# Performance work log

Hardware: AMD Instinct MI355X
Metric: run time of the kernel (lower is better)

The kernel has to match this reference:

```python
import jax, jax.numpy as jnp
import numpy as np
from jax import lax

SIZE = 64
N_PHASES = SIZE * (SIZE - 1) // 2  # 2016
LOSS_DB_CM = 0.5
INSERTION_LOSS_DB = LOSS_DB_CM * 0.1          # per-MZI insertion loss (dB)
LOSS_AMP = 10.0 ** (-INSERTION_LOSS_DB / 20.0)  # amplitude transmission per MZI
NONLINEAR_COEFF = 2.6e-20

# Reck triangular mesh ordering: layer i = 1..SIZE-1, MZIs on adjacent modes (j, j+1)
_MODE_IDX = np.array([j for i in range(1, SIZE) for j in range(i)], dtype=np.int32)


def build_mesh_unitary(phases):
    """Sequentially compose 2x2 MZI rotations into a SIZE x SIZE complex matrix.
    Each MZI with phase theta applies T = loss * [[cos, i sin],[i sin, cos]] to
    adjacent modes (m, m+1). U = T_K ... T_1."""
    U0 = jnp.eye(SIZE, dtype=jnp.complex64)

    def step(U, xs):
        theta, m = xs
        c = jnp.cos(theta).astype(jnp.complex64)
        s = (1j * jnp.sin(theta)).astype(jnp.complex64)
        row_a = U[m]
        row_b = U[m + 1]
        new_a = LOSS_AMP * (c * row_a + s * row_b)
        new_b = LOSS_AMP * (s * row_a + c * row_b)
        U = U.at[m].set(new_a).at[m + 1].set(new_b)
        return U, None

    U, _ = lax.scan(step, U0, (phases, jnp.asarray(_MODE_IDX)))
    return U


def setup_inputs() -> dict:
    key = jax.random.key(0)
    k1, k2, k3 = jax.random.split(key, 3)
    B = 262144
    x_real = jax.random.normal(k1, (B, SIZE), dtype=jnp.float32)
    x_imag = jax.random.normal(k2, (B, SIZE), dtype=jnp.float32)
    # nn.initializers.uniform(scale=2*pi) -> U[0, 2*pi)
    phases = jax.random.uniform(k3, (N_PHASES,), dtype=jnp.float32) * (2.0 * np.pi)
    return {"x_real": x_real, "x_imag": x_imag, "phases": phases}


def reference(x_real, x_imag, phases):
    x = (x_real + 1j * x_imag).astype(jnp.complex64)  # [B, SIZE]
    U = build_mesh_unitary(phases)                    # [SIZE, SIZE] complex64
    # vmapped mesh apply == batched matmul with the composed unitary
    out = x @ U.T                                     # [B, SIZE]
    # Kerr nonlinearity (include_nonlinearity=True)
    optical_power = jnp.abs(out) ** 2
    nonlinear_phase = NONLINEAR_COEFF * optical_power * 1000.0
    out = out * jnp.exp(1j * nonlinear_phase.astype(jnp.complex64))
    return out
```

## Files before the change

kernel.cpp:

```cpp
#include <hip/hip_runtime.h>


#define PSIZE 64
#define N_PHASES 2016
#define NLAYER 63
#define LOSS_AMP 0.99426007f
#define NL_COEFF 2.6e-17f

#define UF32_BYTES (2 * PSIZE * PSIZE * 4)
#define WSPLIT_BYTES (4 * PSIZE * PSIZE * 2)
#define WS_NEED (UF32_BYTES + WSPLIT_BYTES)

typedef __attribute__((ext_vector_type(8))) short sh8;
typedef __attribute__((ext_vector_type(4))) float f32x4;

__device__ __align__(16) float g_U_fallback[2 * PSIZE * PSIZE];

__device__ inline unsigned short f32_to_bf16_rn(float f) {
  unsigned int u = __float_as_uint(f);
  u += 0x7fffu + ((u >> 16) & 1u);
  return (unsigned short)(u >> 16);
}
__device__ inline float bf16_to_f32(unsigned short h) {
  return __uint_as_float(((unsigned int)h) << 16);
}

__device__ inline float rdlane(float v, int l) {
  return __int_as_float(__builtin_amdgcn_readlane(__float_as_int(v), l));
}

__device__ inline unsigned pkbf16(float a, float b) {
  unsigned r;
  asm("v_cvt_pk_bf16_f32 %0, %1, %2" : "=v"(r) : "v"(a), "v"(b));
  return r;
}
__device__ inline float lo16f(unsigned u) { return __uint_as_float(u << 16); }
__device__ inline float hi16f(unsigned u) {
  return __uint_as_float(u & 0xFFFF0000u);
}
__device__ inline sh8 mk8(unsigned a, unsigned b, unsigned c, unsigned d) {
  union { unsigned u[4]; sh8 s; } t;
  t.u[0] = a; t.u[1] = b; t.u[2] = c; t.u[3] = d;
  return t.s;
}

__global__ __launch_bounds__(512, 1) void build_kernel(
    const float* __restrict__ phases,
    float* __restrict__ Uf32,
    unsigned short* __restrict__ Wout) {
  __shared__ float2 sS[3][PSIZE * PSIZE];
  __shared__ float2 sWsm[PSIZE * PSIZE];
  const int tid = threadIdx.x;
  const int wv = tid >> 6;
  const int lane = tid & 63;

  for (int idx = tid; idx < PSIZE * PSIZE; idx += 512) {
    const int li = idx >> 6;
    const int m = idx & 63;
    float2 w = make_float2(1.0f, 0.0f);
    if (li < NLAYER && m <= li) {
      const float th = phases[(li * (li + 1)) / 2 + m];
      w = make_float2(LOSS_AMP * cosf(th), LOSS_AMP * sinf(th));
    }
    sWsm[idx] = w;
  }
  __syncthreads();

  float ure[PSIZE], uim[PSIZE];
  if (wv < 4) {
#pragma unroll
    for (int r = 0; r < PSIZE; ++r) {
      ure[r] = (r == lane) ? 1.0f : 0.0f;
      uim[r] = 0.0f;
    }
    for (int l = 0; l < 16; ++l) {
      const int li = wv * 16 + l;
      const float2 w2 = sWsm[li * 64 + lane];
#pragma unroll
      for (int m = 0; m < NLAYER; ++m) {
        const float wc = rdlane(w2.x, m);
        const float ws = rdlane(w2.y, m);
        const float are = ure[m], aim = uim[m];
        const float bre = ure[m + 1], bim = uim[m + 1];
        ure[m]     = fmaf(wc, are, -ws * bim);
        uim[m]     = fmaf(wc, aim,  ws * bre);
        ure[m + 1] = fmaf(wc, bre, -ws * aim);
        uim[m + 1] = fmaf(wc, bim,  ws * are);
      }
    }
  }
  __syncthreads();

  if (wv < 4) {
    float2* dst = (wv == 3) ? sWsm : sS[wv];
#pragma unroll
    for (int r = 0; r < PSIZE; ++r)
      dst[r * 64 + lane] = make_float2(ure[r], uim[r]);
  }
  __syncthreads();

  const int wg = wv >> 2;
  const int w4 = wv & 3;
  {
    const float2* A  = (wg == 0) ? sS[1] : sWsm;
    const float2* Bm = (wg == 0) ? sS[0] : sS[2];
    float pre[16], pim[16];
#pragma unroll
    for (int r = 0; r < 16; ++r) { pre[r] = 0.f; pim[r] = 0.f; }
    for (int m = 0; m < PSIZE; ++m) {
      const float2 b = Bm[m * 64 + lane];
#pragma unroll
      for (int r = 0; r < 16; ++r) {
        const float2 a = A[(16 * w4 + r) * 64 + m];
        pre[r] = fmaf(a.x, b.x, fmaf(-a.y, b.y, pre[r]));
        pim[r] = fmaf(a.x, b.y, fmaf( a.y, b.x, pim[r]));
      }
    }
    __syncthreads();
    float2* Pd = (wg == 0) ? sS[0] : sS[1];
#pragma unroll
    for (int r = 0; r < 16; ++r)
      Pd[(16 * w4 + r) * 64 + lane] = make_float2(pre[r], pim[r]);
  }
  __syncthreads();

  float fre[8], fim[8];
#pragma unroll
  for (int r = 0; r < 8; ++r) { fre[r] = 0.f; fim[r] = 0.f; }
  for (int m = 0; m < PSIZE; ++m) {
    const float2 b = sS[0][m * 64 + lane];
#pragma unroll
    for (int r = 0; r < 8; ++r) {
      const float2 a = sS[1][(8 * wv + r) * 64 + m];
      fre[r] = fmaf(a.x, b.x, fmaf(-a.y, b.y, fre[r]));
      fim[r] = fmaf(a.x, b.y, fmaf( a.y, b.x, fim[r]));
    }
  }

  float* Udst = (Uf32 != nullptr) ? Uf32 : g_U_fallback;
#pragma unroll
  for (int r = 0; r < 8; ++r) {
    const int rr = 8 * wv + r;
    ((float2*)Udst)[rr * 64 + lane] = make_float2(fre[r], fim[r]);
  }
  if (Wout != nullptr) {
    const int slot = lane >> 3, kin = lane & 7;
#pragma unroll
    for (int r = 0; r < 8; ++r) {
      const int n = 8 * wv + r;
      const int base = n * 64 + ((slot ^ (n & 7)) << 3) + kin;
      const unsigned short rh = f32_to_bf16_rn(fre[r]);
      const unsigned short rl = f32_to_bf16_rn(fre[r] - bf16_to_f32(rh));
      const unsigned short ih = f32_to_bf16_rn(fim[r]);
      const unsigned short il = f32_to_bf16_rn(fim[r] - bf16_to_f32(ih));
      Wout[0 * 4096 + base] = rh;
      Wout[1 * 4096 + base] = rl;
      Wout[2 * 4096 + base] = ih;
      Wout[3 * 4096 + base] = il;
    }
  }
}

__global__ __launch_bounds__(256, 2) void apply_mfma(
    const unsigned short* __restrict__ W,
    const float* __restrict__ xr,
    const float* __restrict__ xi,
    float* __restrict__ out_re,
    float* __restrict__ out_im) {
  __shared__ __align__(16) unsigned short sW[4 * PSIZE * PSIZE];
  {
    const float4* src = (const float4*)W;
    float4* dst = (float4*)sW;
    for (int i = threadIdx.x; i < WSPLIT_BYTES / 16; i += 256) dst[i] = src[i];
  }
  __syncthreads();

  const int lane = threadIdx.x & 63;
  const int wave = threadIdx.x >> 6;
  const int lm = lane & 15;
  const int lg = lane >> 4;
  const long row0 = (long)blockIdx.x * 128 + (long)wave * 32;

  f32x4 accRe[2][4], accIm[2][4];
#pragma unroll
  for (int a = 0; a < 2; ++a)
#pragma unroll
    for (int b = 0; b < 4; ++b) {
      accRe[a][b] = f32x4{0.f, 0.f, 0.f, 0.f};
      accIm[a][b] = f32x4{0.f, 0.f, 0.f, 0.f};
    }

#pragma unroll
  for (int ks = 0; ks < 2; ++ks) {
    sh8 arh[2], arl[2], aih[2], ail[2], anh[2], anl[2];
#pragma unroll
    for (int mt = 0; mt < 2; ++mt) {
      const long r = row0 + mt * 16 + lm;
      const float4* pr = (const float4*)(xr + r * PSIZE + ks * 32 + lg * 8);
      const float4* pi = (const float4*)(xi + r * PSIZE + ks * 32 + lg * 8);
      const float4 v0 = pr[0], v1 = pr[1];
      const float4 w0 = pi[0], w1 = pi[1];

      const unsigned rh0 = pkbf16(v0.x, v0.y), rh1 = pkbf16(v0.z, v0.w);
      const unsigned rh2 = pkbf16(v1.x, v1.y), rh3 = pkbf16(v1.z, v1.w);
      const unsigned rl0 = pkbf16(v0.x - lo16f(rh0), v0.y - hi16f(rh0));
      const unsigned rl1 = pkbf16(v0.z - lo16f(rh1), v0.w - hi16f(rh1));
      const unsigned rl2 = pkbf16(v1.x - lo16f(rh2), v1.y - hi16f(rh2));
      const unsigned rl3 = pkbf16(v1.z - lo16f(rh3), v1.w - hi16f(rh3));
      arh[mt] = mk8(rh0, rh1, rh2, rh3);
      arl[mt] = mk8(rl0, rl1, rl2, rl3);

      const unsigned ih0 = pkbf16(w0.x, w0.y), ih1 = pkbf16(w0.z, w0.w);
      const unsigned ih2 = pkbf16(w1.x, w1.y), ih3 = pkbf16(w1.z, w1.w);
      const unsigned il0 = pkbf16(w0.x - lo16f(ih0), w0.y - hi16f(ih0));
      const unsigned il1 = pkbf16(w0.z - lo16f(ih1), w0.w - hi16f(ih1));
      const unsigned il2 = pkbf16(w1.x - lo16f(ih2), w1.y - hi16f(ih2));
      const unsigned il3 = pkbf16(w1.z - lo16f(ih3), w1.w - hi16f(ih3));
      aih[mt] = mk8(ih0, ih1, ih2, ih3);
      ail[mt] = mk8(il0, il1, il2, il3);
      anh[mt] = mk8(ih0 ^ 0x80008000u, ih1 ^ 0x80008000u,
                    ih2 ^ 0x80008000u, ih3 ^ 0x80008000u);
      anl[mt] = mk8(il0 ^ 0x80008000u, il1 ^ 0x80008000u,
                    il2 ^ 0x80008000u, il3 ^ 0x80008000u);
    }

#pragma unroll
    for (int nt = 0; nt < 4; ++nt) {
      const int n = nt * 16 + lm;
      const int sidx = n * 64 + (((ks * 4 + lg) ^ (n & 7)) << 3);
      const sh8 bRh = *(const sh8*)&sW[0 * 4096 + sidx];
      const sh8 bRl = *(const sh8*)&sW[1 * 4096 + sidx];
      const sh8 bIh = *(const sh8*)&sW[2 * 4096 + sidx];
      const sh8 bIl = *(const sh8*)&sW[3 * 4096 + sidx];
#pragma unroll
      for (int mt = 0; mt < 2; ++mt) {
        f32x4 cr = accRe[mt][nt];
        cr = __builtin_amdgcn_mfma_f32_16x16x32_bf16(arh[mt], bRh, cr, 0, 0, 0);
        cr = __builtin_amdgcn_mfma_f32_16x16x32_bf16(arh[mt], bRl, cr, 0, 0, 0);
        cr = __builtin_amdgcn_mfma_f32_16x16x32_bf16(arl[mt], bRh, cr, 0, 0, 0);
        cr = __builtin_amdgcn_mfma_f32_16x16x32_bf16(anh[mt], bIh, cr, 0, 0, 0);
        cr = __builtin_amdgcn_mfma_f32_16x16x32_bf16(anh[mt], bIl, cr, 0, 0, 0);
        cr = __builtin_amdgcn_mfma_f32_16x16x32_bf16(anl[mt], bIh, cr, 0, 0, 0);
        accRe[mt][nt] = cr;
        f32x4 ci = accIm[mt][nt];
        ci = __builtin_amdgcn_mfma_f32_16x16x32_bf16(arh[mt], bIh, ci, 0, 0, 0);
        ci = __builtin_amdgcn_mfma_f32_16x16x32_bf16(arh[mt], bIl, ci, 0, 0, 0);
        ci = __builtin_amdgcn_mfma_f32_16x16x32_bf16(arl[mt], bIh, ci, 0, 0, 0);
        ci = __builtin_amdgcn_mfma_f32_16x16x32_bf16(aih[mt], bRh, ci, 0, 0, 0);
        ci = __builtin_amdgcn_mfma_f32_16x16x32_bf16(aih[mt], bRl, ci, 0, 0, 0);
        ci = __builtin_amdgcn_mfma_f32_16x16x32_bf16(ail[mt], bRh, ci, 0, 0, 0);
        accIm[mt][nt] = ci;
      }
    }
  }

#pragma unroll
  for (int mt = 0; mt < 2; ++mt) {
#pragma unroll
    for (int reg = 0; reg < 4; ++reg) {
      const long row = row0 + mt * 16 + lg * 4 + reg;
#pragma unroll
      for (int nt = 0; nt < 4; ++nt) {
        const int col = nt * 16 + lm;
        const float re = accRe[mt][nt][reg];
        const float im = accIm[mt][nt][reg];
        const float p = NL_COEFF * fmaf(re, re, im * im);
        out_re[row * PSIZE + col] = fmaf(-im, p, re);
        if (out_im != nullptr) out_im[row * PSIZE + col] = fmaf(re, p, im);
      }
    }
  }
}

__global__ __launch_bounds__(256, 2) void tail_kernel(
    const float* __restrict__ Usrc,
    const float* __restrict__ xr,
    const float* __restrict__ xi,
    float* __restrict__ out_re,
    float* __restrict__ out_im,
    long rowStart, long nrows) {
  __shared__ __align__(16) float sU[2 * PSIZE * PSIZE];
  {
    const float4* g4 = (const float4*)((Usrc != nullptr) ? Usrc : g_U_fallback);
    float4* s4 = (float4*)sU;
    for (int i = threadIdx.x; i < (2 * PSIZE * PSIZE) / 4; i += 256)
      s4[i] = g4[i];
  }
  __syncthreads();

  const long row = rowStart + (long)blockIdx.x * 256 + threadIdx.x;
  if (row >= nrows) return;

  const float4* xr4 = (const float4*)(xr + (size_t)row * PSIZE);
  const float4* xi4 = (const float4*)(xi + (size_t)row * PSIZE);

  float aR[PSIZE], aI[PSIZE];
#pragma unroll
  for (int j = 0; j < PSIZE; ++j) { aR[j] = 0.0f; aI[j] = 0.0f; }

  const float4* su4 = (const float4*)sU;

#pragma unroll 1
  for (int kc = 0; kc < 8; ++kc) {
    const float4 a0 = xr4[2 * kc];
    const float4 a1 = xr4[2 * kc + 1];
    const float4 b0 = xi4[2 * kc];
    const float4 b1 = xi4[2 * kc + 1];
    const float4* up = su4 + kc * 4;
#pragma unroll
    for (int j = 0; j < PSIZE; ++j) {
      const float4 u0 = up[j * 32 + 0];
      const float4 u1 = up[j * 32 + 1];
      const float4 u2 = up[j * 32 + 2];
      const float4 u3 = up[j * 32 + 3];
      float r = aR[j], m = aI[j];
      r = fmaf(a0.x, u0.x, r); r = fmaf(-b0.x, u0.y, r);
      m = fmaf(a0.x, u0.y, m); m = fmaf( b0.x, u0.x, m);
      r = fmaf(a0.y, u0.z, r); r = fmaf(-b0.y, u0.w, r);
      m = fmaf(a0.y, u0.w, m); m = fmaf( b0.y, u0.z, m);
      r = fmaf(a0.z, u1.x, r); r = fmaf(-b0.z, u1.y, r);
      m = fmaf(a0.z, u1.y, m); m = fmaf( b0.z, u1.x, m);
      r = fmaf(a0.w, u1.z, r); r = fmaf(-b0.w, u1.w, r);
      m = fmaf(a0.w, u1.w, m); m = fmaf( b0.w, u1.z, m);
      r = fmaf(a1.x, u2.x, r); r = fmaf(-b1.x, u2.y, r);
      m = fmaf(a1.x, u2.y, m); m = fmaf( b1.x, u2.x, m);
      r = fmaf(a1.y, u2.z, r); r = fmaf(-b1.y, u2.w, r);
      m = fmaf(a1.y, u2.w, m); m = fmaf( b1.y, u2.z, m);
      r = fmaf(a1.z, u3.x, r); r = fmaf(-b1.z, u3.y, r);
      m = fmaf(a1.z, u3.y, m); m = fmaf( b1.z, u3.x, m);
      r = fmaf(a1.w, u3.z, r); r = fmaf(-b1.w, u3.w, r);
      m = fmaf(a1.w, u3.w, m); m = fmaf( b1.w, u3.z, m);
      aR[j] = r; aI[j] = m;
    }
  }

  float* orp = out_re + (size_t)row * PSIZE;
  float* oip = (out_im != nullptr) ? (out_im + (size_t)row * PSIZE) : nullptr;
#pragma unroll
  for (int jq = 0; jq < 16; ++jq) {
    const int j = 4 * jq;
    float4 vr, vi;
    {
      const float p = NL_COEFF * fmaf(aR[j], aR[j], aI[j] * aI[j]);
      vr.x = fmaf(-aI[j], p, aR[j]); vi.x = fmaf(aR[j], p, aI[j]);
    }
    {
      const float p = NL_COEFF * fmaf(aR[j+1], aR[j+1], aI[j+1] * aI[j+1]);
      vr.y = fmaf(-aI[j+1], p, aR[j+1]); vi.y = fmaf(aR[j+1], p, aI[j+1]);
    }
    {
      const float p = NL_COEFF * fmaf(aR[j+2], aR[j+2], aI[j+2] * aI[j+2]);
      vr.z = fmaf(-aI[j+2], p, aR[j+2]); vi.z = fmaf(aR[j+2], p, aI[j+2]);
    }
    {
      const float p = NL_COEFF * fmaf(aR[j+3], aR[j+3], aI[j+3] * aI[j+3]);
      vr.w = fmaf(-aI[j+3], p, aR[j+3]); vi.w = fmaf(aR[j+3], p, aI[j+3]);
    }
    ((float4*)orp)[jq] = vr;
    if (oip != nullptr) ((float4*)oip)[jq] = vi;
  }
}

extern "C" void kernel_launch(void* const* d_in, const int* in_sizes, int n_in,
                              void* d_out, int out_size, void* d_ws, size_t ws_size,
                              hipStream_t stream) {
  int pidx = -1;
  for (int i = 0; i < n_in; ++i) {
    if (in_sizes[i] == N_PHASES) { pidx = i; break; }
  }
  if (pidx < 0) pidx = 2;
  int xa = -1, xb = -1;
  for (int i = 0; i < n_in; ++i) {
    if (i == pidx) continue;
    if (xa < 0) xa = i;
    else if (xb < 0) xb = i;
  }
  if (xa < 0 || xb < 0) return;

  const float* phases = (const float*)d_in[pidx];
  const float* x_real = (const float*)d_in[xa];
  const float* x_imag = (const float*)d_in[xb];

  long b_in = (long)in_sizes[xa] / PSIZE;
  if ((long)in_sizes[xb] / PSIZE < b_in) b_in = (long)in_sizes[xb] / PSIZE;

  float* out = (float*)d_out;
  float* out_re = out;
  float* out_im = nullptr;
  long nrows;

  if ((long)out_size >= 2 * b_in * PSIZE) {
    const long half = (long)out_size / 2;
    out_im = out + half;
    long cap = half / PSIZE;
    nrows = (b_in < cap) ? b_in : cap;
  } else {
    long cap = (long)out_size / PSIZE;
    nrows = (b_in < cap) ? b_in : cap;
  }
  if (nrows <= 0) return;

  float* Uf32 = nullptr;
  unsigned short* Wsplit = nullptr;
  if (d_ws != nullptr && ws_size >= (size_t)WS_NEED) {
    Uf32 = (float*)d_ws;
    Wsplit = (unsigned short*)((char*)d_ws + UF32_BYTES);
  }

  build_kernel<<<1, 512, 0, stream>>>(phases, Uf32, Wsplit);

  const long ntiles = (Wsplit != nullptr) ? (nrows / 128) : 0;
  if (ntiles > 0) {
    apply_mfma<<<(int)ntiles, 256, 0, stream>>>(Wsplit, x_real, x_imag,
                                                out_re, out_im);
  }
  const long done = ntiles * 128;
  if (done < nrows) {
    const long rem = nrows - done;
    const int tblocks = (int)((rem + 255) / 256);
    tail_kernel<<<tblocks, 256, 0, stream>>>(Uf32, x_real, x_imag,
                                             out_re, out_im, done, nrows);
  }
}
```

Baseline: 231.7 us.

## Fuse unitary build into apply kernel with ticket-based producer/consumer handoff

Replaces the separate single-block build kernel and the MFMA apply kernel with one persistent-style launch. The first block to take a ticket builds the unitary, publishes the split bf16 weights through global memory with a release flag, then does its own tile. All other blocks spin on the flag before loading the weights. This removes a kernel launch boundary and the serial gap before apply starts. In exchange it adds a memset, spin-waiting blocks that occupy CUs while the build runs, and a reliance on the ticket holder being scheduled.

```diff
diff --git a/kernel.cpp b/kernel.cpp
--- a/kernel.cpp
+++ b/kernel.cpp
@@ -7,9 +7,9 @@
 #define LOSS_AMP 0.99426007f
 #define NL_COEFF 2.6e-17f
 
-#define UF32_BYTES (2 * PSIZE * PSIZE * 4)
 #define WSPLIT_BYTES (4 * PSIZE * PSIZE * 2)
-#define WS_NEED (UF32_BYTES + WSPLIT_BYTES)
+#define CTRL_BYTES 256
+#define FUSED_WS_NEED (CTRL_BYTES + WSPLIT_BYTES)
 
 typedef __attribute__((ext_vector_type(8))) short sh8;
 typedef __attribute__((ext_vector_type(4))) float f32x4;
@@ -24,11 +24,9 @@
 __device__ inline float bf16_to_f32(unsigned short h) {
   return __uint_as_float(((unsigned int)h) << 16);
 }
-
 __device__ inline float rdlane(float v, int l) {
   return __int_as_float(__builtin_amdgcn_readlane(__float_as_int(v), l));
 }
-
 __device__ inline unsigned pkbf16(float a, float b) {
   unsigned r;
   asm("v_cvt_pk_bf16_f32 %0, %1, %2" : "=v"(r) : "v"(a), "v"(b));
@@ -44,38 +42,46 @@
   return t.s;
 }
 
-__global__ __launch_bounds__(512, 1) void build_kernel(
+__global__ __launch_bounds__(256, 2) void fused_kernel(
     const float* __restrict__ phases,
-    float* __restrict__ Uf32,
-    unsigned short* __restrict__ Wout) {
-  __shared__ float2 sS[3][PSIZE * PSIZE];
-  __shared__ float2 sWsm[PSIZE * PSIZE];
+    const float* __restrict__ xr,
+    const float* __restrict__ xi,
+    float* __restrict__ out_re,
+    float* __restrict__ out_im,
+    unsigned* __restrict__ ctrl,
+    unsigned short* __restrict__ Wg,
+    long nrows) {
+  __shared__ __align__(16) float2 sA[PSIZE * PSIZE];
+  __shared__ __align__(16) float2 sB[PSIZE * PSIZE];
+  __shared__ unsigned s_ticket;
+  unsigned short* sW = (unsigned short*)sA;
+
   const int tid = threadIdx.x;
-  const int wv = tid >> 6;
-  const int lane = tid & 63;
-
-  for (int idx = tid; idx < PSIZE * PSIZE; idx += 512) {
-    const int li = idx >> 6;
-    const int m = idx & 63;
-    float2 w = make_float2(1.0f, 0.0f);
-    if (li < NLAYER && m <= li) {
-      const float th = phases[(li * (li + 1)) / 2 + m];
-      w = make_float2(LOSS_AMP * cosf(th), LOSS_AMP * sinf(th));
-    }
-    sWsm[idx] = w;
-  }
+  if (tid == 0) s_ticket = atomicAdd(&ctrl[0], 1u);
   __syncthreads();
 
-  float ure[PSIZE], uim[PSIZE];
-  if (wv < 4) {
+  if (s_ticket == 0) {
+    const int wv = tid >> 6, lane = tid & 63;
+
+    for (int idx = tid; idx < PSIZE * PSIZE; idx += 256) {
+      const int li = idx >> 6, m = idx & 63;
+      float2 w = make_float2(1.0f, 0.0f);
+      if (li < NLAYER && m <= li) {
+        const float th = phases[(li * (li + 1)) / 2 + m];
+        w = make_float2(LOSS_AMP * cosf(th), LOSS_AMP * sinf(th));
+      }
+      sA[idx] = w;
+    }
+    __syncthreads();
+
+    float ure[PSIZE], uim[PSIZE];
 #pragma unroll
     for (int r = 0; r < PSIZE; ++r) {
       ure[r] = (r == lane) ? 1.0f : 0.0f;
       uim[r] = 0.0f;
     }
     for (int l = 0; l < 16; ++l) {
-      const int li = wv * 16 + l;
-      const float2 w2 = sWsm[li * 64 + lane];
+      const float2 w2 = sA[(wv * 16 + l) * 64 + lane];
 #pragma unroll
       for (int m = 0; m < NLAYER; ++m) {
         const float wc = rdlane(w2.x, m);
@@ -88,92 +94,122 @@
         uim[m + 1] = fmaf(wc, bim,  ws * are);
       }
     }
-  }
-  __syncthreads();
-
-  if (wv < 4) {
-    float2* dst = (wv == 3) ? sWsm : sS[wv];
-#pragma unroll
-    for (int r = 0; r < PSIZE; ++r)
-      dst[r * 64 + lane] = make_float2(ure[r], uim[r]);
-  }
-  __syncthreads();
-
-  const int wg = wv >> 2;
-  const int w4 = wv & 3;
-  {
-    const float2* A  = (wg == 0) ? sS[1] : sWsm;
-    const float2* Bm = (wg == 0) ? sS[0] : sS[2];
+    __syncthreads();
+
+    if (wv == 3) {
+#pragma unroll
+      for (int r = 0; r < PSIZE; ++r)
+        ((float2*)Wg)[r * 64 + lane] = make_float2(ure[r], uim[r]);
+    }
+    if (wv == 0) {
+#pragma unroll
+      for (int r = 0; r < PSIZE; ++r)
+        sA[r * 64 + lane] = make_float2(ure[r], uim[r]);
+    }
+    if (wv == 1) {
+#pragma unroll
+      for (int r = 0; r < PSIZE; ++r)
+        sB[r * 64 + lane] = make_float2(ure[r], uim[r]);
+    }
+    __syncthreads();
+
     float pre[16], pim[16];
 #pragma unroll
     for (int r = 0; r < 16; ++r) { pre[r] = 0.f; pim[r] = 0.f; }
     for (int m = 0; m < PSIZE; ++m) {
-      const float2 b = Bm[m * 64 + lane];
+      const float2 b = sA[m * 64 + lane];
 #pragma unroll
       for (int r = 0; r < 16; ++r) {
-        const float2 a = A[(16 * w4 + r) * 64 + m];
+        const float2 a = sB[(wv * 16 + r) * 64 + m];
         pre[r] = fmaf(a.x, b.x, fmaf(-a.y, b.y, pre[r]));
         pim[r] = fmaf(a.x, b.y, fmaf( a.y, b.x, pim[r]));
       }
     }
     __syncthreads();
-    float2* Pd = (wg == 0) ? sS[0] : sS[1];
+    if (wv == 2) {
+#pragma unroll
+      for (int r = 0; r < PSIZE; ++r)
+        sA[r * 64 + lane] = make_float2(ure[r], uim[r]);
+    }
 #pragma unroll
     for (int r = 0; r < 16; ++r)
-      Pd[(16 * w4 + r) * 64 + lane] = make_float2(pre[r], pim[r]);
-  }
-  __syncthreads();
-
-  float fre[8], fim[8];
-#pragma unroll
-  for (int r = 0; r < 8; ++r) { fre[r] = 0.f; fim[r] = 0.f; }
-  for (int m = 0; m < PSIZE; ++m) {
-    const float2 b = sS[0][m * 64 + lane];
-#pragma unroll
-    for (int r = 0; r < 8; ++r) {
-      const float2 a = sS[1][(8 * wv + r) * 64 + m];
-      fre[r] = fmaf(a.x, b.x, fmaf(-a.y, b.y, fre[r]));
-      fim[r] = fmaf(a.x, b.y, fmaf( a.y, b.x, fim[r]));
-    }
-  }
-
-  float* Udst = (Uf32 != nullptr) ? Uf32 : g_U_fallback;
-#pragma unroll
-  for (int r = 0; r < 8; ++r) {
-    const int rr = 8 * wv + r;
-    ((float2*)Udst)[rr * 64 + lane] = make_float2(fre[r], fim[r]);
-  }
-  if (Wout != nullptr) {
+      sB[(wv * 16 + r) * 64 + lane] = make_float2(pre[r], pim[r]);
+    __syncthreads();
+
+#pragma unroll
+    for (int r = 0; r < 16; ++r) { pre[r] = 0.f; pim[r] = 0.f; }
+    for (int m = 0; m < PSIZE; ++m) {
+      const float2 b = sB[m * 64 + lane];
+#pragma unroll
+      for (int r = 0; r < 16; ++r) {
+        const float2 a = sA[(wv * 16 + r) * 64 + m];
+        pre[r] = fmaf(a.x, b.x, fmaf(-a.y, b.y, pre[r]));
+        pim[r] = fmaf(a.x, b.y, fmaf( a.y, b.x, pim[r]));
+      }
+    }
+    __syncthreads();
+#pragma unroll
+    for (int r = 0; r < 16; ++r)
+      sB[(wv * 16 + r) * 64 + lane] = make_float2(pre[r], pim[r]);
+    for (int idx = tid; idx < PSIZE * PSIZE; idx += 256)
+      sA[idx] = ((const float2*)Wg)[idx];
+    __syncthreads();
+
+    float fre[16], fim[16];
+#pragma unroll
+    for (int r = 0; r < 16; ++r) { fre[r] = 0.f; fim[r] = 0.f; }
+    for (int m = 0; m < PSIZE; ++m) {
+      const float2 b = sB[m * 64 + lane];
+#pragma unroll
+      for (int r = 0; r < 16; ++r) {
+        const float2 a = sA[(wv * 16 + r) * 64 + m];
+        fre[r] = fmaf(a.x, b.x, fmaf(-a.y, b.y, fre[r]));
+        fim[r] = fmaf(a.x, b.y, fmaf( a.y, b.x, fim[r]));
+      }
+    }
+    __syncthreads();
+
     const int slot = lane >> 3, kin = lane & 7;
 #pragma unroll
-    for (int r = 0; r < 8; ++r) {
-      const int n = 8 * wv + r;
+    for (int r = 0; r < 16; ++r) {
+      const int n = wv * 16 + r;
       const int base = n * 64 + ((slot ^ (n & 7)) << 3) + kin;
       const unsigned short rh = f32_to_bf16_rn(fre[r]);
       const unsigned short rl = f32_to_bf16_rn(fre[r] - bf16_to_f32(rh));
       const unsigned short ih = f32_to_bf16_rn(fim[r]);
       const unsigned short il = f32_to_bf16_rn(fim[r] - bf16_to_f32(ih));
-      Wout[0 * 4096 + base] = rh;
-      Wout[1 * 4096 + base] = rl;
-      Wout[2 * 4096 + base] = ih;
-      Wout[3 * 4096 + base] = il;
-    }
-  }
-}
-
-__global__ __launch_bounds__(256, 2) void apply_mfma(
-    const unsigned short* __restrict__ W,
-    const float* __restrict__ xr,
-    const float* __restrict__ xi,
-    float* __restrict__ out_re,
-    float* __restrict__ out_im) {
-  __shared__ __align__(16) unsigned short sW[4 * PSIZE * PSIZE];
-  {
-    const float4* src = (const float4*)W;
-    float4* dst = (float4*)sW;
-    for (int i = threadIdx.x; i < WSPLIT_BYTES / 16; i += 256) dst[i] = src[i];
-  }
-  __syncthreads();
+      sW[0 * 4096 + base] = rh;
+      sW[1 * 4096 + base] = rl;
+      sW[2 * 4096 + base] = ih;
+      sW[3 * 4096 + base] = il;
+    }
+    __syncthreads();
+    {
+      const float4* s4 = (const float4*)sW;
+      float4* d4 = (float4*)Wg;
+      for (int i = tid; i < WSPLIT_BYTES / 16; i += 256) d4[i] = s4[i];
+    }
+    __syncthreads();
+    __threadfence();
+    if (tid == 0)
+      __hip_atomic_store(&ctrl[1], 1u, __ATOMIC_RELEASE,
+                         __HIP_MEMORY_SCOPE_AGENT);
+  } else {
+    if (tid == 0) {
+      while (__hip_atomic_load(&ctrl[1], __ATOMIC_RELAXED,
+                               __HIP_MEMORY_SCOPE_AGENT) == 0u)
+        __builtin_amdgcn_s_sleep(16);
+    }
+    __syncthreads();
+    (void)__hip_atomic_load(&ctrl[1], __ATOMIC_ACQUIRE,
+                            __HIP_MEMORY_SCOPE_AGENT);
+    {
+      const float4* src = (const float4*)Wg;
+      float4* dst = (float4*)sW;
+      for (int i = tid; i < WSPLIT_BYTES / 16; i += 256) dst[i] = src[i];
+    }
+    __syncthreads();
+  }
 
   const int lane = threadIdx.x & 63;
   const int wave = threadIdx.x >> 6;
@@ -195,7 +231,8 @@
     sh8 arh[2], arl[2], aih[2], ail[2], anh[2], anl[2];
 #pragma unroll
     for (int mt = 0; mt < 2; ++mt) {
-      const long r = row0 + mt * 16 + lm;
+      long r = row0 + mt * 16 + lm;
+      if (r >= nrows) r = nrows - 1;
       const float4* pr = (const float4*)(xr + r * PSIZE + ks * 32 + lg * 8);
       const float4* pi = (const float4*)(xi + r * PSIZE + ks * 32 + lg * 8);
       const float4 v0 = pr[0], v1 = pr[1];
@@ -259,36 +296,129 @@
 #pragma unroll
     for (int reg = 0; reg < 4; ++reg) {
       const long row = row0 + mt * 16 + lg * 4 + reg;
-#pragma unroll
-      for (int nt = 0; nt < 4; ++nt) {
-        const int col = nt * 16 + lm;
-        const float re = accRe[mt][nt][reg];
-        const float im = accIm[mt][nt][reg];
-        const float p = NL_COEFF * fmaf(re, re, im * im);
-        out_re[row * PSIZE + col] = fmaf(-im, p, re);
-        if (out_im != nullptr) out_im[row * PSIZE + col] = fmaf(re, p, im);
-      }
-    }
-  }
+      if (row < nrows) {
+#pragma unroll
+        for (int nt = 0; nt < 4; ++nt) {
+          const int col = nt * 16 + lm;
+          const float re = accRe[mt][nt][reg];
+          const float im = accIm[mt][nt][reg];
+          const float p = NL_COEFF * fmaf(re, re, im * im);
+          out_re[row * PSIZE + col] = fmaf(-im, p, re);
+          if (out_im != nullptr) out_im[row * PSIZE + col] = fmaf(re, p, im);
+        }
+      }
+    }
+  }
+}
+
+__global__ __launch_bounds__(512, 1) void build_kernel(
+    const float* __restrict__ phases) {
+  __shared__ float2 sS[3][PSIZE * PSIZE];
+  __shared__ float2 sWsm[PSIZE * PSIZE];
+  const int tid = threadIdx.x;
+  const int wv = tid >> 6;
+  const int lane = tid & 63;
+
+  for (int idx = tid; idx < PSIZE * PSIZE; idx += 512) {
+    const int li = idx >> 6, m = idx & 63;
+    float2 w = make_float2(1.0f, 0.0f);
+    if (li < NLAYER && m <= li) {
+      const float th = phases[(li * (li + 1)) / 2 + m];
+      w = make_float2(LOSS_AMP * cosf(th), LOSS_AMP * sinf(th));
+    }
+    sWsm[idx] = w;
+  }
+  __syncthreads();
+
+  float ure[PSIZE], uim[PSIZE];
+  if (wv < 4) {
+#pragma unroll
+    for (int r = 0; r < PSIZE; ++r) {
+      ure[r] = (r == lane) ? 1.0f : 0.0f;
+      uim[r] = 0.0f;
+    }
+    for (int l = 0; l < 16; ++l) {
+      const float2 w2 = sWsm[(wv * 16 + l) * 64 + lane];
+#pragma unroll
+      for (int m = 0; m < NLAYER; ++m) {
+        const float wc = rdlane(w2.x, m);
+        const float ws = rdlane(w2.y, m);
+        const float are = ure[m], aim = uim[m];
+        const float bre = ure[m + 1], bim = uim[m + 1];
+        ure[m]     = fmaf(wc, are, -ws * bim);
+        uim[m]     = fmaf(wc, aim,  ws * bre);
+        ure[m + 1] = fmaf(wc, bre, -ws * aim);
+        uim[m + 1] = fmaf(wc, bim,  ws * are);
+      }
+    }
+  }
+  __syncthreads();
+  if (wv < 4) {
+    float2* dst = (wv == 3) ? sWsm : sS[wv];
+#pragma unroll
+    for (int r = 0; r < PSIZE; ++r)
+      dst[r * 64 + lane] = make_float2(ure[r], uim[r]);
+  }
+  __syncthreads();
+
+  const int wg = wv >> 2, w4 = wv & 3;
+  {
+    const float2* A  = (wg == 0) ? sS[1] : sWsm;
+    const float2* Bm = (wg == 0) ? sS[0] : sS[2];
+    float pre[16], pim[16];
+#pragma unroll
+    for (int r = 0; r < 16; ++r) { pre[r] = 0.f; pim[r] = 0.f; }
+    for (int m = 0; m < PSIZE; ++m) {
+      const float2 b = Bm[m * 64 + lane];
+#pragma unroll
+      for (int r = 0; r < 16; ++r) {
+        const float2 a = A[(16 * w4 + r) * 64 + m];
+        pre[r] = fmaf(a.x, b.x, fmaf(-a.y, b.y, pre[r]));
+        pim[r] = fmaf(a.x, b.y, fmaf( a.y, b.x, pim[r]));
+      }
+    }
+    __syncthreads();
+    float2* Pd = (wg == 0) ? sS[0] : sS[1];
+#pragma unroll
+    for (int r = 0; r < 16; ++r)
+      Pd[(16 * w4 + r) * 64 + lane] = make_float2(pre[r], pim[r]);
+  }
+  __syncthreads();
+
+  float fre[8], fim[8];
+#pragma unroll
+  for (int r = 0; r < 8; ++r) { fre[r] = 0.f; fim[r] = 0.f; }
+  for (int m = 0; m < PSIZE; ++m) {
+    const float2 b = sS[0][m * 64 + lane];
+#pragma unroll
+    for (int r = 0; r < 8; ++r) {
+      const float2 a = sS[1][(8 * wv + r) * 64 + m];
+      fre[r] = fmaf(a.x, b.x, fmaf(-a.y, b.y, fre[r]));
+      fim[r] = fmaf(a.x, b.y, fmaf( a.y, b.x, fim[r]));
+    }
+  }
+#pragma unroll
+  for (int r = 0; r < 8; ++r)
+    ((float2*)g_U_fallback)[(8 * wv + r) * 64 + lane] =
+        make_float2(fre[r], fim[r]);
 }
 
 __global__ __launch_bounds__(256, 2) void tail_kernel(
-    const float* __restrict__ Usrc,
     const float* __restrict__ xr,
     const float* __restrict__ xi,
     float* __restrict__ out_re,
     float* __restrict__ out_im,
-    long rowStart, long nrows) {
+    long nrows) {
   __shared__ __align__(16) float sU[2 * PSIZE * PSIZE];
   {
-    const float4* g4 = (const float4*)((Usrc != nullptr) ? Usrc : g_U_fallback);
+    const float4* g4 = (const float4*)g_U_fallback;
     float4* s4 = (float4*)sU;
     for (int i = threadIdx.x; i < (2 * PSIZE * PSIZE) / 4; i += 256)
       s4[i] = g4[i];
   }
   __syncthreads();
 
-  const long row = rowStart + (long)blockIdx.x * 256 + threadIdx.x;
+  const long row = (long)blockIdx.x * 256 + threadIdx.x;
   if (row >= nrows) return;
 
   const float4* xr4 = (const float4*)(xr + (size_t)row * PSIZE);
@@ -400,25 +530,17 @@
   }
   if (nrows <= 0) return;
 
-  float* Uf32 = nullptr;
-  unsigned short* Wsplit = nullptr;
-  if (d_ws != nullptr && ws_size >= (size_t)WS_NEED) {
-    Uf32 = (float*)d_ws;
-    Wsplit = (unsigned short*)((char*)d_ws + UF32_BYTES);
-  }
-
-  build_kernel<<<1, 512, 0, stream>>>(phases, Uf32, Wsplit);
-
-  const long ntiles = (Wsplit != nullptr) ? (nrows / 128) : 0;
-  if (ntiles > 0) {
-    apply_mfma<<<(int)ntiles, 256, 0, stream>>>(Wsplit, x_real, x_imag,
-                                                out_re, out_im);
-  }
-  const long done = ntiles * 128;
-  if (done < nrows) {
-    const long rem = nrows - done;
-    const int tblocks = (int)((rem + 255) / 256);
-    tail_kernel<<<tblocks, 256, 0, stream>>>(Uf32, x_real, x_imag,
-                                             out_re, out_im, done, nrows);
-  }
-}
+  if (d_ws != nullptr && ws_size >= (size_t)FUSED_WS_NEED) {
+    hipMemsetAsync(d_ws, 0, CTRL_BYTES, stream);
+    unsigned* ctrl = (unsigned*)d_ws;
+    unsigned short* Wg = (unsigned short*)((char*)d_ws + CTRL_BYTES);
+    const int nblocks = (int)((nrows + 127) / 128);
+    fused_kernel<<<nblocks, 256, 0, stream>>>(phases, x_real, x_imag,
+                                              out_re, out_im, ctrl, Wg, nrows);
+  } else {
+    build_kernel<<<1, 512, 0, stream>>>(phases);
+    const int tblocks = (int)((nrows + 255) / 256);
+    tail_kernel<<<tblocks, 256, 0, stream>>>(x_real, x_imag,
+                                             out_re, out_im, nrows);
+  }
+}
```

Result: slower. 352.4 us (+52.1%).
